# Performance work log

Measured on AMD Instinct MI355X. Metric: run time of the kernel, lower is better.

The kernel has to match this reference:

```python
import jax, jax.numpy as jnp
import numpy as np
from jax import lax
from math import sqrt

STYLE_DIM = 512
K = 3


def _equal_linear(latent, w, b):
    # EqualLinear: runtime weight scaling by 1/sqrt(fan_in)
    scale = 1.0 / sqrt(latent.shape[1])
    return latent @ (w.T * scale) + b


def _pixel_norm(x, axis=1, eps=1e-8):
    return x * jax.lax.rsqrt(jnp.mean(x * x, axis=axis, keepdims=True) + eps)


def _modconv(x, latent, weight, bias, el_w, el_b):
    # weight: (nc2, nc1, 3, 3); x: (B, nc1, H, W); latent: (B, style_dim)
    b = x.shape[0]
    nc2, nc1, k, _ = weight.shape
    fan_in = nc1 * k * k
    w = weight * sqrt(2.0 / fan_in)                      # (nc2, nc1, 3, 3)
    # style: s = 1 + PixelNorm(EqualLinear(latent))      # (B, nc1)
    s = 1.0 + _pixel_norm(_equal_linear(latent, el_w, el_b), axis=1)
    # demod: d_bo = rsqrt(sum_{c,k} (s_bc * w_ock)^2 + 1e-5)
    wsq = jnp.sum(w * w, axis=(2, 3))                    # (nc2, nc1)
    d = jax.lax.rsqrt(jnp.einsum('bc,oc->bo', s * s, wsq) + 1e-5)  # (B, nc2)
    # conv(x, s*w)*d  ==  conv(s*x, w)*d  (s is per input channel)
    xm = x * s[:, :, None, None]
    y = lax.conv_general_dilated(
        xm, w, window_strides=(1, 1), padding=[(1, 1), (1, 1)],
        dimension_numbers=('NCHW', 'OIHW', 'NCHW'))
    return y * d[:, :, None, None] + bias


def _style_block(x, latent, w0, b0, el0_w, el0_b, w1, b1, el1_w, el1_b):
    act_gain = sqrt(2.0)
    out = _modconv(x, latent, w0, b0, el0_w, el0_b)
    out = jax.nn.leaky_relu(out, 0.2) * act_gain
    out = _pixel_norm(out, axis=1)
    out = _modconv(out, latent, w1, b1, el1_w, el1_b)
    out = jax.nn.leaky_relu(out, 0.2) * act_gain
    out = _pixel_norm(out, axis=1)
    return out


def setup_inputs() -> dict:
    key = jax.random.key(0)
    ks = jax.random.split(key, 8)
    B, NC1, NC2, H, W = 8, 256, 256, 128, 128
    return {
        'x': jax.random.normal(ks[0], (B, NC1, H, W), jnp.float32),
        'latent': jax.random.normal(ks[1], (B, STYLE_DIM), jnp.float32),
        'w0': jax.random.normal(ks[2], (NC2, NC1, K, K), jnp.float32),
        'b0': jnp.zeros((1, NC2, 1, 1), jnp.float32),
        'el0_w': jax.random.normal(ks[3], (NC1, STYLE_DIM), jnp.float32),
        'el0_b': jnp.zeros((NC1,), jnp.float32),
        'w1': jax.random.normal(ks[4], (NC2, NC2, K, K), jnp.float32),
        'b1': jnp.zeros((1, NC2, 1, 1), jnp.float32),
        'el1_w': jax.random.normal(ks[5], (NC2, STYLE_DIM), jnp.float32),
        'el1_b': jnp.zeros((NC2,), jnp.float32),
    }


def reference(x, latent, w0, b0, el0_w, el0_b, w1, b1, el1_w, el1_b):
    return _style_block(x, latent, w0, b0, el0_w, el0_b, w1, b1, el1_w, el1_b)
```

## Files before the change

kernel.cpp:

```cpp
#include <hip/hip_runtime.h>
#include <hip/hip_bf16.h>

typedef __attribute__((ext_vector_type(8))) short short8;
typedef __attribute__((ext_vector_type(16))) float f32x16;

typedef const __attribute__((address_space(1))) unsigned int* gas1_t;
typedef __attribute__((address_space(3))) unsigned int* las3_t;

__device__ __forceinline__ unsigned short f2bf(float x) {
    unsigned int u = __float_as_uint(x);
    u = (u + 0x7fffu + ((u >> 16) & 1u)) >> 16;
    return (unsigned short)u;
}

__device__ __forceinline__ int4 pack8(const unsigned short* u) {
    int4 p;
    p.x = (int)((unsigned)u[0] | ((unsigned)u[1] << 16));
    p.y = (int)((unsigned)u[2] | ((unsigned)u[3] << 16));
    p.z = (int)((unsigned)u[4] | ((unsigned)u[5] << 16));
    p.w = (int)((unsigned)u[6] | ((unsigned)u[7] << 16));
    return p;
}

__device__ __forceinline__ void gld_lds16(const void* g, void* l) {
    __builtin_amdgcn_global_load_lds((gas1_t)g, (las3_t)l, 16, 0, 0);
}

__global__ void style_kernel(const float* __restrict__ latent,
                             const float* __restrict__ elw0, const float* __restrict__ elb0,
                             const float* __restrict__ elw1, const float* __restrict__ elb1,
                             float* __restrict__ s_arr) {
    const int cv = blockIdx.x >> 3;
    const int b  = blockIdx.x & 7;
    const int c  = threadIdx.x;
    const float* elw = cv ? elw1 : elw0;
    const float* elb = cv ? elb1 : elb0;

    __shared__ float lat[512];
    lat[c] = latent[b * 512 + c];
    lat[c + 256] = latent[b * 512 + c + 256];
    __syncthreads();

    float accv = 0.f;
    const float* wrow = elw + (size_t)c * 512;
#pragma unroll 8
    for (int k = 0; k < 512; ++k) accv += lat[k] * wrow[k];
    const float lin = accv * 0.04419417382415922f + elb[c];

    float sq = lin * lin;
#pragma unroll
    for (int off = 32; off >= 1; off >>= 1) sq += __shfl_xor(sq, off);
    __shared__ float wsum[4];
    if ((threadIdx.x & 63) == 0) wsum[threadIdx.x >> 6] = sq;
    __syncthreads();
    const float total = wsum[0] + wsum[1] + wsum[2] + wsum[3];
    const float s = 1.0f + lin * rsqrtf(total * (1.0f / 256.0f) + 1e-8f);
    s_arr[(cv * 8 + b) * 256 + c] = s;
}

__global__ void wsq_kernel(const float* __restrict__ w0, const float* __restrict__ w1,
                           float* __restrict__ wsq) {
    const int cv = blockIdx.x >> 8;
    const int o  = blockIdx.x & 255;
    const int c  = threadIdx.x;
    const float* w = cv ? w1 : w0;
    const size_t base = ((size_t)o * 256 + c) * 9;
    float ssum = 0.f;
#pragma unroll
    for (int t = 0; t < 9; ++t) { float v = w[base + t]; ssum += v * v; }
    wsq[((size_t)cv * 256 + o) * 256 + c] = ssum * (2.0f / 2304.0f);
}

__global__ void demod_kernel(const float* __restrict__ s_arr, const float* __restrict__ wsq,
                             float* __restrict__ d_arr) {
    const int cv = blockIdx.x >> 3;
    const int b  = blockIdx.x & 7;
    const int o  = threadIdx.x;
    __shared__ float ss[256];
    float sv = s_arr[(cv * 8 + b) * 256 + o];
    ss[o] = sv * sv;
    __syncthreads();
    const float* wrow = wsq + ((size_t)cv * 256 + o) * 256;
    float accv = 0.f;
#pragma unroll 8
    for (int c = 0; c < 256; ++c) accv += ss[c] * wrow[c];
    d_arr[(cv * 8 + b) * 256 + o] = rsqrtf(accv + 1e-5f);
}

__global__ void fold_kernel(const float* __restrict__ w0, const float* __restrict__ w1,
                            const float* __restrict__ s_arr, const float* __restrict__ d_arr,
                            unsigned short* __restrict__ wm0, unsigned short* __restrict__ wm1) {
    const int cv = blockIdx.y;
    const int e  = blockIdx.x * 256 + threadIdx.x;
    const float* w = cv ? w1 : w0;
    unsigned short* wm = cv ? wm1 : wm0;
    const int slab = e >> 13;
    const int idx  = e & 8191;
    const int b  = slab / 72;
    const int s2 = slab - b * 72;
    const int cc = s2 / 9;
    const int t  = s2 - cc * 9;
    const int o  = idx >> 5;
    const int c5 = idx & 31;
    const int c  = cc * 32 + c5;
    const float val = w[((size_t)o * 256 + c) * 9 + t] * 0.029462782549439483f
                    * s_arr[(cv * 8 + b) * 256 + c] * d_arr[(cv * 8 + b) * 256 + o];
    const int chunk = (c5 >> 3) ^ ((o >> 1) & 3);
    wm[((size_t)slab << 13) + o * 32 + (chunk << 3) + (c5 & 7)] = f2bf(val);
}

__global__ void convert_kernel(const float* __restrict__ x, unsigned short* __restrict__ xq) {
    const int blk = blockIdx.x;
    const int hh  = blk & 127;
    const int bg_ = blk >> 7;
    const int g   = bg_ & 31;
    const int b   = bg_ >> 5;
    __shared__ float sx[8][128];
    const int tid = threadIdx.x;
#pragma unroll
    for (int i = 0; i < 4; ++i) {
        const int idx = tid + i * 256;
        const int c8 = idx >> 7, p = idx & 127;
        sx[c8][p] = x[(((size_t)b * 256 + g * 8 + c8) * 128 + hh) * 128 + p];
    }
    __syncthreads();
    if (tid < 128) {
        const int p = tid;
        unsigned short u[8];
#pragma unroll
        for (int j = 0; j < 8; ++j) u[j] = f2bf(sx[j][p]);
        *(int4*)(xq + ((((size_t)b * 32 + g) * 128 + hh) * 128 + p) * 8) = pack8(u);
    }
}

template<bool FINAL_OUT>
__global__ __launch_bounds__(256, 2) void conv_kernel(
    const unsigned short* __restrict__ in_q, const unsigned short* __restrict__ wmod,
    const float* __restrict__ bias, const unsigned short* __restrict__ zpg,
    void* __restrict__ out_v) {

    __shared__ __align__(16) char ldsA[49152];
    __shared__ __align__(16) char ldsB[24640];
    __shared__ float sbias[256];

    const int tid  = threadIdx.x;
    const int bh   = (blockIdx.x & 7) * 128 + (blockIdx.x >> 3);
    const int b    = bh >> 7;
    const int h    = bh & 127;
    const int lane = tid & 63;
    const int wr   = tid >> 6;
    const int wm   = wr & 1;
    const int wn   = wr >> 1;
    const int l31  = lane & 31;
    const int khg  = lane >> 5;

    sbias[tid] = bias[tid];
    if (tid < 4) *(int4*)(ldsB + 24576 + tid * 16) = (int4){0, 0, 0, 0};

    int aoff[4][2];
#pragma unroll
    for (int mb = 0; mb < 4; ++mb)
#pragma unroll
        for (int kh = 0; kh < 2; ++kh) {
            const int o = wm * 128 + mb * 32 + l31;
            aoff[mb][kh] = o * 64 + (((khg + kh * 2) ^ ((o >> 1) & 3)) << 4);
        }

    int bC[2][2], bL[2][2], bR[2][2];
#pragma unroll
    for (int nb = 0; nb < 2; ++nb)
#pragma unroll
        for (int kh = 0; kh < 2; ++kh) {
            const int cx0 = wn * 64 + nb * 32 + l31;
            const int clog = khg + kh * 2;
            const int cl = cx0 - 1, cr = cx0 + 1;
            bC[nb][kh] = cx0 * 64 + ((clog ^ ((cx0 >> 1) & 3)) << 4);
            bL[nb][kh] = cl * 64 + ((clog ^ ((cl >> 1) & 3)) << 4);
            bR[nb][kh] = cr * 64 + ((clog ^ ((cr >> 1) & 3)) << 4);
        }
    const bool isL = (wn == 0) && (l31 == 0);
    const bool isR = (wn == 1) && (l31 == 31);

    const unsigned short* wmb = wmod + (size_t)b * 589824;
    const unsigned short* xqb = in_q + (size_t)b * 4194304;

    auto issueA = [&](const char* src, int bufidx) {
        char* dstb = ldsA + bufidx * 16384 + wr * 1024;
        const char* s = src + wr * 1024 + lane * 16;
#pragma unroll
        for (int i = 0; i < 4; ++i)
            gld_lds16(s + i * 4096, dstb + i * 4096);
    };

    auto issueB = [&](int ccn) {
#pragma unroll
        for (int i = 0; i < 6; ++i) {
            const int slot = i * 256 + tid;
            const int rowidx = slot >> 2;
            const int cph = slot & 3;
            const int r = rowidx >> 7;
            const int pxs = rowidx & 127;
            const int clog = cph ^ ((rowidx >> 1) & 3);
            const int hin = h + r - 1;
            const unsigned short* src = ((unsigned)hin < 128u)
                ? xqb + (((size_t)(ccn * 4 + clog) * 128 + hin) * 128 + pxs) * 8
                : zpg;
            gld_lds16(src, ldsB + (i * 256 + wr * 64) * 16);
        }
    };

    f32x16 acc[4][2];
#pragma unroll
    for (int mb = 0; mb < 4; ++mb)
#pragma unroll
        for (int nb = 0; nb < 2; ++nb)
#pragma unroll
            for (int r = 0; r < 16; ++r) acc[mb][nb][r] = 0.f;

    issueB(0);
    issueA((const char*)wmb, 0);
    issueA((const char*)wmb + 16384, 1);
    __syncthreads();

    const char* gA = (const char*)wmb + 32768;
#pragma unroll 1
    for (int cc = 0; cc < 8; ++cc) {
#pragma unroll
        for (int t = 0; t < 9; ++t) {
            const int dy = t / 3, dx = t - (t / 3) * 3;
            const int cur = t % 3, tgt = (t + 2) % 3;
            const bool doIssue = (cc < 7) || (t < 7);
            if (doIssue) { issueA(gA, tgt); gA += 16384; }

            const char* Ac = ldsA + cur * 16384;
            short8 af[4][2], bf[2][2];
#pragma unroll
            for (int mb = 0; mb < 4; ++mb)
#pragma unroll
                for (int kh = 0; kh < 2; ++kh) af[mb][kh] = *(const short8*)(Ac + aoff[mb][kh]);
#pragma unroll
            for (int nb = 0; nb < 2; ++nb)
#pragma unroll
                for (int kh = 0; kh < 2; ++kh) {
                    int off;
                    if (dx == 1) {
                        off = bC[nb][kh] + dy * 8192;
                    } else if (dx == 0) {
                        off = bL[nb][kh] + dy * 8192;
                        if (nb == 0) off = isL ? 24576 : off;
                    } else {
                        off = bR[nb][kh] + dy * 8192;
                        if (nb == 1) off = isR ? 24576 : off;
                    }
                    bf[nb][kh] = *(const short8*)(ldsB + off);
                }

            __builtin_amdgcn_s_setprio(1);
#pragma unroll
            for (int kh = 0; kh < 2; ++kh)
#pragma unroll
                for (int mb = 0; mb < 4; ++mb)
#pragma unroll
                    for (int nb = 0; nb < 2; ++nb)
                        acc[mb][nb] = __builtin_amdgcn_mfma_f32_32x32x16_bf16(
                            af[mb][kh], bf[nb][kh], acc[mb][nb], 0, 0, 0);
            __builtin_amdgcn_s_setprio(0);

            if (doIssue) asm volatile("s_waitcnt vmcnt(4) lgkmcnt(0)" ::: "memory");
            else         asm volatile("s_waitcnt vmcnt(0) lgkmcnt(0)" ::: "memory");
            __builtin_amdgcn_sched_barrier(0);
            __builtin_amdgcn_s_barrier();
        }
        if (cc < 7) {
            issueB(cc + 1);
            __syncthreads();
        }
    }

    float psum[2] = {0.f, 0.f};
    const float actGain = 1.4142135623730951f;
#pragma unroll
    for (int mb = 0; mb < 4; ++mb)
#pragma unroll
        for (int rg = 0; rg < 16; ++rg) {
            const int row = (rg & 3) + 8 * (rg >> 2) + 4 * khg;
            const float bo = sbias[wm * 128 + mb * 32 + row];
#pragma unroll
            for (int nb = 0; nb < 2; ++nb) {
                float v = acc[mb][nb][rg] + bo;
                v = (v > 0.f ? v : 0.2f * v) * actGain;
                acc[mb][nb][rg] = v;
                psum[nb] += v * v;
            }
        }
    psum[0] += __shfl_xor(psum[0], 32);
    psum[1] += __shfl_xor(psum[1], 32);
    float* red = (float*)ldsA;
    if (lane < 32) {
        red[(wn * 2 + wm) * 64 + l31]      = psum[0];
        red[(wn * 2 + wm) * 64 + 32 + l31] = psum[1];
    }
    __syncthreads();
    float rs[2];
#pragma unroll
    for (int nb = 0; nb < 2; ++nb) {
        const float ssum = red[(wn * 2) * 64 + nb * 32 + l31]
                         + red[(wn * 2 + 1) * 64 + nb * 32 + l31];
        rs[nb] = rsqrtf(ssum * (1.0f / 256.0f) + 1e-8f);
    }

    if (FINAL_OUT) {
        float* outF = (float*)out_v;
#pragma unroll
        for (int mb = 0; mb < 4; ++mb)
#pragma unroll
            for (int rg = 0; rg < 16; ++rg) {
                const int row = (rg & 3) + 8 * (rg >> 2) + 4 * khg;
                const int o = wm * 128 + mb * 32 + row;
                const size_t rb = (((size_t)b * 256 + o) * 128 + h) * 128;
#pragma unroll
                for (int nb = 0; nb < 2; ++nb)
                    outF[rb + wn * 64 + nb * 32 + l31] = acc[mb][nb][rg] * rs[nb];
            }
    } else {
        unsigned short* outB = (unsigned short*)out_v;
        char* wreg = ldsA + wr * 4096;
        __syncthreads();
#pragma unroll
        for (int mb = 0; mb < 4; ++mb) {
#pragma unroll
            for (int rg = 0; rg < 16; rg += 2) {
                const int row = (rg & 3) + 8 * (rg >> 2) + 4 * khg;
#pragma unroll
                for (int nb = 0; nb < 2; ++nb) {
                    const int pxl = nb * 32 + l31;
                    const unsigned lo = f2bf(acc[mb][nb][rg]     * rs[nb]);
                    const unsigned hi = f2bf(acc[mb][nb][rg + 1] * rs[nb]);
                    *(unsigned int*)(wreg + pxl * 64 + (((row >> 3) ^ (pxl & 3)) << 4)
                                     + (row & 7) * 2) = lo | (hi << 16);
                }
            }
            asm volatile("s_waitcnt lgkmcnt(0)" ::: "memory");
#pragma unroll
            for (int oc = 0; oc < 4; ++oc) {
                const int4 v = *(const int4*)(wreg + lane * 64 + ((oc ^ (lane & 3)) << 4));
                const int g = wm * 16 + mb * 4 + oc;
                *(int4*)(outB + ((((size_t)b * 32 + g) * 128 + h) * 128 + wn * 64 + lane) * 8) = v;
            }
            asm volatile("s_waitcnt lgkmcnt(0)" ::: "memory");
        }
    }
}

extern "C" void kernel_launch(void* const* d_in, const int* in_sizes, int n_in,
                              void* d_out, int out_size, void* d_ws, size_t ws_size,
                              hipStream_t stream) {
    (void)in_sizes; (void)n_in; (void)out_size; (void)ws_size;
    const float* x      = (const float*)d_in[0];
    const float* latent = (const float*)d_in[1];
    const float* w0     = (const float*)d_in[2];
    const float* b0     = (const float*)d_in[3];
    const float* el0w   = (const float*)d_in[4];
    const float* el0b   = (const float*)d_in[5];
    const float* w1     = (const float*)d_in[6];
    const float* b1     = (const float*)d_in[7];
    const float* el1w   = (const float*)d_in[8];
    const float* el1b   = (const float*)d_in[9];

    char* ws = (char*)d_ws;
    float* s_arr = (float*)ws;
    float* d_arr = (float*)(ws + 16384);
    float* wsq   = (float*)(ws + 32768);
    unsigned short* zpg = (unsigned short*)(ws + 32768);
    unsigned short* wm0 = (unsigned short*)(ws + 557056);
    unsigned short* wm1 = (unsigned short*)(ws + 9994240);
    unsigned short* xq  = (unsigned short*)(ws + 19431424);
    unsigned short* tmp = (unsigned short*)(ws + 86540288);

    style_kernel<<<16, 256, 0, stream>>>(latent, el0w, el0b, el1w, el1b, s_arr);
    wsq_kernel<<<512, 256, 0, stream>>>(w0, w1, wsq);
    demod_kernel<<<16, 256, 0, stream>>>(s_arr, wsq, d_arr);
    hipMemsetAsync(zpg, 0, 256, stream);
    fold_kernel<<<dim3(18432, 2), 256, 0, stream>>>(w0, w1, s_arr, d_arr, wm0, wm1);
    convert_kernel<<<32768, 256, 0, stream>>>(x, xq);

    conv_kernel<false><<<1024, 256, 0, stream>>>(xq, wm0, b0, zpg, tmp);
    conv_kernel<true><<<1024, 256, 0, stream>>>(tmp, wm1, b1, zpg, d_out);
}
```

Measured before the change: 398.5 us.

## Process two output rows per block with 512 threads to reuse weight tiles

Each conv block now computes two image rows (256 channels x 256 pixels) with 8 waves instead of one row with 4 waves, so every modulated-weight slab loaded into LDS serves twice as many pixels and weight traffic from global memory is halved. The weight layout in the fold kernel changes from a per-row XOR swizzle to a chunk-major layout, and the input halo staging now loads four rows with simpler addressing. Blocks use more LDS (about 87KB) and twice the threads, which may cut occupancy and the number of blocks per CU, and the grid drops to 512 blocks.

```diff
diff --git a/kernel.cpp b/kernel.cpp
--- a/kernel.cpp
+++ b/kernel.cpp
@@ -105,8 +105,7 @@
     const int c  = cc * 32 + c5;
     const float val = w[((size_t)o * 256 + c) * 9 + t] * 0.029462782549439483f
                     * s_arr[(cv * 8 + b) * 256 + c] * d_arr[(cv * 8 + b) * 256 + o];
-    const int chunk = (c5 >> 3) ^ ((o >> 1) & 3);
-    wm[((size_t)slab << 13) + o * 32 + (chunk << 3) + (c5 & 7)] = f2bf(val);
+    wm[((size_t)slab << 13) + (c5 >> 3) * 2048 + o * 8 + (c5 & 7)] = f2bf(val);
 }
 
 __global__ void convert_kernel(const float* __restrict__ x, unsigned short* __restrict__ xq) {
@@ -134,86 +133,62 @@
 }
 
 template<bool FINAL_OUT>
-__global__ __launch_bounds__(256, 2) void conv_kernel(
+__global__ __launch_bounds__(512, 2) void conv_kernel(
     const unsigned short* __restrict__ in_q, const unsigned short* __restrict__ wmod,
     const float* __restrict__ bias, const unsigned short* __restrict__ zpg,
     void* __restrict__ out_v) {
 
-    __shared__ __align__(16) char ldsA[49152];
-    __shared__ __align__(16) char ldsB[24640];
-    __shared__ float sbias[256];
+    __shared__ __align__(16) char lds[87104];
 
     const int tid  = threadIdx.x;
-    const int bh   = (blockIdx.x & 7) * 128 + (blockIdx.x >> 3);
-    const int b    = bh >> 7;
-    const int h    = bh & 127;
+    const int b    = blockIdx.x & 7;
+    const int rp   = blockIdx.x >> 3;
+    const int h0   = rp * 2;
     const int lane = tid & 63;
     const int wr   = tid >> 6;
-    const int wm   = wr & 1;
-    const int wn   = wr >> 1;
+    const int wm   = wr & 3;
+    const int wn   = wr >> 2;
     const int l31  = lane & 31;
     const int khg  = lane >> 5;
 
-    sbias[tid] = bias[tid];
-    if (tid < 4) *(int4*)(ldsB + 24576 + tid * 16) = (int4){0, 0, 0, 0};
-
-    int aoff[4][2];
-#pragma unroll
-    for (int mb = 0; mb < 4; ++mb)
-#pragma unroll
-        for (int kh = 0; kh < 2; ++kh) {
-            const int o = wm * 128 + mb * 32 + l31;
-            aoff[mb][kh] = o * 64 + (((khg + kh * 2) ^ ((o >> 1) & 3)) << 4);
-        }
-
-    int bC[2][2], bL[2][2], bR[2][2];
-#pragma unroll
-    for (int nb = 0; nb < 2; ++nb)
-#pragma unroll
-        for (int kh = 0; kh < 2; ++kh) {
-            const int cx0 = wn * 64 + nb * 32 + l31;
-            const int clog = khg + kh * 2;
-            const int cl = cx0 - 1, cr = cx0 + 1;
-            bC[nb][kh] = cx0 * 64 + ((clog ^ ((cx0 >> 1) & 3)) << 4);
-            bL[nb][kh] = cl * 64 + ((clog ^ ((cl >> 1) & 3)) << 4);
-            bR[nb][kh] = cr * 64 + ((clog ^ ((cr >> 1) & 3)) << 4);
-        }
-    const bool isL = (wn == 0) && (l31 == 0);
-    const bool isR = (wn == 1) && (l31 == 31);
+    float* sbias = (float*)(lds + 81984);
+    if (tid < 256) sbias[tid] = bias[tid];
+    if (tid < 4)   *(int4*)(lds + 81920 + tid * 16) = (int4){0, 0, 0, 0};
+
+    int aoff[2][2];
+#pragma unroll
+    for (int mb = 0; mb < 2; ++mb)
+#pragma unroll
+        for (int kh = 0; kh < 2; ++kh)
+            aoff[mb][kh] = ((khg + 2 * kh) * 256 + wm * 64 + mb * 32 + l31) * 16;
 
     const unsigned short* wmb = wmod + (size_t)b * 589824;
     const unsigned short* xqb = in_q + (size_t)b * 4194304;
 
-    auto issueA = [&](const char* src, int bufidx) {
-        char* dstb = ldsA + bufidx * 16384 + wr * 1024;
-        const char* s = src + wr * 1024 + lane * 16;
-#pragma unroll
-        for (int i = 0; i < 4; ++i)
-            gld_lds16(s + i * 4096, dstb + i * 4096);
+    auto issueA = [&](const char* src, int buf) {
+        char* db = lds + buf * 16384 + wr * 2048;
+        const char* s = src + wr * 2048 + lane * 16;
+        gld_lds16(s,        db);
+        gld_lds16(s + 1024, db + 1024);
     };
 
-    auto issueB = [&](int ccn) {
-#pragma unroll
-        for (int i = 0; i < 6; ++i) {
-            const int slot = i * 256 + tid;
-            const int rowidx = slot >> 2;
-            const int cph = slot & 3;
-            const int r = rowidx >> 7;
-            const int pxs = rowidx & 127;
-            const int clog = cph ^ ((rowidx >> 1) & 3);
-            const int hin = h + r - 1;
+    auto issueB = [&](int cc) {
+        const int chunk = tid >> 7, px = tid & 127;
+#pragma unroll
+        for (int r = 0; r < 4; ++r) {
+            const int hin = h0 - 1 + r;
             const unsigned short* src = ((unsigned)hin < 128u)
-                ? xqb + (((size_t)(ccn * 4 + clog) * 128 + hin) * 128 + pxs) * 8
+                ? xqb + (((size_t)(cc * 4 + chunk) * 128 + hin) * 128 + px) * 8
                 : zpg;
-            gld_lds16(src, ldsB + (i * 256 + wr * 64) * 16);
+            gld_lds16(src, lds + 49152 + r * 8192 + wr * 1024);
         }
     };
 
-    f32x16 acc[4][2];
-#pragma unroll
-    for (int mb = 0; mb < 4; ++mb)
-#pragma unroll
-        for (int nb = 0; nb < 2; ++nb)
+    f32x16 acc[2][4];
+#pragma unroll
+    for (int mb = 0; mb < 2; ++mb)
+#pragma unroll
+        for (int nb = 0; nb < 4; ++nb)
 #pragma unroll
             for (int r = 0; r < 16; ++r) acc[mb][nb][r] = 0.f;
 
@@ -229,110 +204,109 @@
         for (int t = 0; t < 9; ++t) {
             const int dy = t / 3, dx = t - (t / 3) * 3;
             const int cur = t % 3, tgt = (t + 2) % 3;
-            const bool doIssue = (cc < 7) || (t < 7);
+            const bool doIssue = (t <= 6) || (cc < 7);
             if (doIssue) { issueA(gA, tgt); gA += 16384; }
 
-            const char* Ac = ldsA + cur * 16384;
-            short8 af[4][2], bf[2][2];
-#pragma unroll
-            for (int mb = 0; mb < 4; ++mb)
-#pragma unroll
-                for (int kh = 0; kh < 2; ++kh) af[mb][kh] = *(const short8*)(Ac + aoff[mb][kh]);
-#pragma unroll
-            for (int nb = 0; nb < 2; ++nb)
+            const char* Ac = lds + cur * 16384;
+            short8 af[2][2], bf[4][2];
+#pragma unroll
+            for (int mb = 0; mb < 2; ++mb)
+#pragma unroll
+                for (int kh = 0; kh < 2; ++kh)
+                    af[mb][kh] = *(const short8*)(Ac + aoff[mb][kh]);
+#pragma unroll
+            for (int nb = 0; nb < 4; ++nb)
 #pragma unroll
                 for (int kh = 0; kh < 2; ++kh) {
-                    int off;
-                    if (dx == 1) {
-                        off = bC[nb][kh] + dy * 8192;
-                    } else if (dx == 0) {
-                        off = bL[nb][kh] + dy * 8192;
-                        if (nb == 0) off = isL ? 24576 : off;
-                    } else {
-                        off = bR[nb][kh] + dy * 8192;
-                        if (nb == 1) off = isR ? 24576 : off;
-                    }
-                    bf[nb][kh] = *(const short8*)(ldsB + off);
+                    int off = 49152 + (wn + dy) * 8192 + (khg + 2 * kh) * 2048
+                            + (nb * 32 + l31 + dx - 1) * 16;
+                    if (dx == 0 && nb == 0) off = (l31 == 0)  ? 81920 : off;
+                    if (dx == 2 && nb == 3) off = (l31 == 31) ? 81920 : off;
+                    bf[nb][kh] = *(const short8*)(lds + off);
                 }
 
             __builtin_amdgcn_s_setprio(1);
 #pragma unroll
             for (int kh = 0; kh < 2; ++kh)
 #pragma unroll
-                for (int mb = 0; mb < 4; ++mb)
-#pragma unroll
-                    for (int nb = 0; nb < 2; ++nb)
+                for (int mb = 0; mb < 2; ++mb)
+#pragma unroll
+                    for (int nb = 0; nb < 4; ++nb)
                         acc[mb][nb] = __builtin_amdgcn_mfma_f32_32x32x16_bf16(
                             af[mb][kh], bf[nb][kh], acc[mb][nb], 0, 0, 0);
             __builtin_amdgcn_s_setprio(0);
 
-            if (doIssue) asm volatile("s_waitcnt vmcnt(4) lgkmcnt(0)" ::: "memory");
+            if (doIssue) asm volatile("s_waitcnt vmcnt(2) lgkmcnt(0)" ::: "memory");
             else         asm volatile("s_waitcnt vmcnt(0) lgkmcnt(0)" ::: "memory");
             __builtin_amdgcn_sched_barrier(0);
             __builtin_amdgcn_s_barrier();
         }
         if (cc < 7) {
             issueB(cc + 1);
-            __syncthreads();
-        }
-    }
-
-    float psum[2] = {0.f, 0.f};
+            asm volatile("s_waitcnt vmcnt(0)" ::: "memory");
+            __builtin_amdgcn_sched_barrier(0);
+            __builtin_amdgcn_s_barrier();
+        }
+    }
+
+    float psum[4] = {0.f, 0.f, 0.f, 0.f};
     const float actGain = 1.4142135623730951f;
 #pragma unroll
-    for (int mb = 0; mb < 4; ++mb)
+    for (int mb = 0; mb < 2; ++mb)
 #pragma unroll
         for (int rg = 0; rg < 16; ++rg) {
             const int row = (rg & 3) + 8 * (rg >> 2) + 4 * khg;
-            const float bo = sbias[wm * 128 + mb * 32 + row];
-#pragma unroll
-            for (int nb = 0; nb < 2; ++nb) {
+            const float bo = sbias[wm * 64 + mb * 32 + row];
+#pragma unroll
+            for (int nb = 0; nb < 4; ++nb) {
                 float v = acc[mb][nb][rg] + bo;
                 v = (v > 0.f ? v : 0.2f * v) * actGain;
                 acc[mb][nb][rg] = v;
                 psum[nb] += v * v;
             }
         }
-    psum[0] += __shfl_xor(psum[0], 32);
-    psum[1] += __shfl_xor(psum[1], 32);
-    float* red = (float*)ldsA;
+#pragma unroll
+    for (int nb = 0; nb < 4; ++nb) psum[nb] += __shfl_xor(psum[nb], 32);
+    float* red = (float*)(lds + 83008);
     if (lane < 32) {
-        red[(wn * 2 + wm) * 64 + l31]      = psum[0];
-        red[(wn * 2 + wm) * 64 + 32 + l31] = psum[1];
-    }
-    __syncthreads();
-    float rs[2];
-#pragma unroll
-    for (int nb = 0; nb < 2; ++nb) {
-        const float ssum = red[(wn * 2) * 64 + nb * 32 + l31]
-                         + red[(wn * 2 + 1) * 64 + nb * 32 + l31];
+#pragma unroll
+        for (int nb = 0; nb < 4; ++nb)
+            red[(wn * 4 + wm) * 128 + nb * 32 + l31] = psum[nb];
+    }
+    __syncthreads();
+    float rs[4];
+#pragma unroll
+    for (int nb = 0; nb < 4; ++nb) {
+        const int p = nb * 32 + l31;
+        const float ssum = red[(wn * 4 + 0) * 128 + p] + red[(wn * 4 + 1) * 128 + p]
+                         + red[(wn * 4 + 2) * 128 + p] + red[(wn * 4 + 3) * 128 + p];
         rs[nb] = rsqrtf(ssum * (1.0f / 256.0f) + 1e-8f);
     }
 
+    const int h = h0 + wn;
     if (FINAL_OUT) {
         float* outF = (float*)out_v;
 #pragma unroll
-        for (int mb = 0; mb < 4; ++mb)
+        for (int mb = 0; mb < 2; ++mb)
 #pragma unroll
             for (int rg = 0; rg < 16; ++rg) {
                 const int row = (rg & 3) + 8 * (rg >> 2) + 4 * khg;
-                const int o = wm * 128 + mb * 32 + row;
+                const int o = wm * 64 + mb * 32 + row;
                 const size_t rb = (((size_t)b * 256 + o) * 128 + h) * 128;
 #pragma unroll
-                for (int nb = 0; nb < 2; ++nb)
-                    outF[rb + wn * 64 + nb * 32 + l31] = acc[mb][nb][rg] * rs[nb];
+                for (int nb = 0; nb < 4; ++nb)
+                    outF[rb + nb * 32 + l31] = acc[mb][nb][rg] * rs[nb];
             }
     } else {
         unsigned short* outB = (unsigned short*)out_v;
-        char* wreg = ldsA + wr * 4096;
-        __syncthreads();
-#pragma unroll
-        for (int mb = 0; mb < 4; ++mb) {
+        char* wreg = lds + wr * 8192;
+#pragma unroll
+        for (int mb = 0; mb < 2; ++mb) {
 #pragma unroll
             for (int rg = 0; rg < 16; rg += 2) {
                 const int row = (rg & 3) + 8 * (rg >> 2) + 4 * khg;
 #pragma unroll
-                for (int nb = 0; nb < 2; ++nb) {
+                for (int nb = 0; nb < 4; ++nb) {
                     const int pxl = nb * 32 + l31;
                     const unsigned lo = f2bf(acc[mb][nb][rg]     * rs[nb]);
                     const unsigned hi = f2bf(acc[mb][nb][rg + 1] * rs[nb]);
@@ -342,11 +316,14 @@
             }
             asm volatile("s_waitcnt lgkmcnt(0)" ::: "memory");
 #pragma unroll
-            for (int oc = 0; oc < 4; ++oc) {
-                const int4 v = *(const int4*)(wreg + lane * 64 + ((oc ^ (lane & 3)) << 4));
-                const int g = wm * 16 + mb * 4 + oc;
-                *(int4*)(outB + ((((size_t)b * 32 + g) * 128 + h) * 128 + wn * 64 + lane) * 8) = v;
-            }
+            for (int oc = 0; oc < 4; ++oc)
+#pragma unroll
+                for (int ph = 0; ph < 2; ++ph) {
+                    const int pxl = ph * 64 + lane;
+                    const int4 v = *(const int4*)(wreg + pxl * 64 + ((oc ^ (pxl & 3)) << 4));
+                    const int g = wm * 8 + mb * 4 + oc;
+                    *(int4*)(outB + ((((size_t)b * 32 + g) * 128 + h) * 128 + pxl) * 8) = v;
+                }
             asm volatile("s_waitcnt lgkmcnt(0)" ::: "memory");
         }
     }
@@ -384,6 +361,6 @@
     fold_kernel<<<dim3(18432, 2), 256, 0, stream>>>(w0, w1, s_arr, d_arr, wm0, wm1);
     convert_kernel<<<32768, 256, 0, stream>>>(x, xq);
 
-    conv_kernel<false><<<1024, 256, 0, stream>>>(xq, wm0, b0, zpg, tmp);
-    conv_kernel<true><<<1024, 256, 0, stream>>>(tmp, wm1, b1, zpg, d_out);
-}
+    conv_kernel<false><<<512, 512, 0, stream>>>(xq, wm0, b0, zpg, tmp);
+    conv_kernel<true><<<512, 512, 0, stream>>>(tmp, wm1, b1, zpg, d_out);
+}
```

After: 367.3 us. 1.08x faster.
